# Kernel tuning notes

Hardware: AMD Instinct MI355X
Metric: run time of the kernel (lower is better)

## Reference

```python
import jax, jax.numpy as jnp
import numpy as np

NEG_INF = -9e15
NEG_SLOPE = 0.2

def setup_inputs() -> dict:
    key = jax.random.key(0)
    k1, k2, k3, k4 = jax.random.split(key, 4)
    N, d_in, d_out = 8192, 256, 256
    x = jax.random.normal(k1, (N, d_in), dtype=jnp.float32)
    adj = jax.random.randint(k2, (N, N), 0, 2).astype(jnp.float32)
    W = jax.random.normal(k3, (d_in, d_out), dtype=jnp.float32) * (1.0 / np.sqrt(d_in))
    a = jax.random.normal(k4, (2 * d_out,), dtype=jnp.float32) * (1.0 / np.sqrt(2 * d_out))
    return {"x": x, "adj": adj, "W": W, "a": a}

def reference(x, adj, W, a):
    d_out = W.shape[1]
    Wh = x @ W                                   # [N, d_out]
    # a([Wh_i || Wh_j]) decomposed: e_ij = <a_src, Wh_i> + <a_dst, Wh_j>
    e_src = Wh @ a[:d_out]                       # [N]
    e_dst = Wh @ a[d_out:]                       # [N]
    e = jax.nn.leaky_relu(e_src[:, None] + e_dst[None, :], NEG_SLOPE)  # [N, N]
    N = Wh.shape[0]
    mask = (adj > 0) | jnp.eye(N, dtype=bool)
    e = jnp.where(mask, e, NEG_INF)
    alpha = jax.nn.softmax(e, axis=1)            # [N, N]
    h = alpha @ Wh                               # [N, d_out]
    return h
```

## Files before the change

kernel.cpp:

```cpp
#include <hip/hip_runtime.h>
#include <stdint.h>

#define N 8192
#define D 256

typedef __attribute__((ext_vector_type(4))) float f32x4;
typedef __attribute__((ext_vector_type(8))) short bf16x8;

__device__ __forceinline__ unsigned short f2bf(float f) {
    unsigned u = __float_as_uint(f);
    u += 0x7fff + ((u >> 16) & 1);
    return (unsigned short)(u >> 16);
}
__device__ __forceinline__ float leaky(float x) {
    return fmaxf(x, 0.f) + 0.2f * fminf(x, 0.f);
}
__device__ __forceinline__ void sync_lds() {
    asm volatile("s_waitcnt lgkmcnt(0)\n\ts_barrier" ::: "memory");
}

#define K1_BM 16
__global__ __launch_bounds__(256) void k1_gemm(const float* __restrict__ x,
                                               const float* __restrict__ W,
                                               float* __restrict__ Wh,
                                               unsigned short* __restrict__ WhT) {
    __shared__ float xsT[32][20];
    const int t = threadIdx.x;
    const int r0 = blockIdx.x * K1_BM;
    float acc[K1_BM];
#pragma unroll
    for (int i = 0; i < K1_BM; ++i) acc[i] = 0.f;

    for (int k0 = 0; k0 < D; k0 += 32) {
        __syncthreads();
        if (t < 128) {
            int r = t >> 3, ks = (t & 7) * 4;
            float4 v = *(const float4*)(x + (size_t)(r0 + r) * D + k0 + ks);
            xsT[ks + 0][r] = v.x; xsT[ks + 1][r] = v.y;
            xsT[ks + 2][r] = v.z; xsT[ks + 3][r] = v.w;
        }
        __syncthreads();
#pragma unroll 8
        for (int kk = 0; kk < 32; ++kk) {
            float wv = W[(size_t)(k0 + kk) * D + t];
#pragma unroll
            for (int rc = 0; rc < K1_BM / 4; ++rc) {
                float4 xv = *(const float4*)&xsT[kk][rc * 4];
                acc[rc * 4 + 0] += xv.x * wv;
                acc[rc * 4 + 1] += xv.y * wv;
                acc[rc * 4 + 2] += xv.z * wv;
                acc[rc * 4 + 3] += xv.w * wv;
            }
        }
    }
#pragma unroll
    for (int r = 0; r < K1_BM; ++r) Wh[(size_t)(r0 + r) * D + t] = acc[r];
    unsigned short pk[K1_BM];
#pragma unroll
    for (int r = 0; r < K1_BM; ++r) pk[r] = f2bf(acc[r]);
    uint4* dst = (uint4*)(WhT + (size_t)t * N + r0);
    dst[0] = *(uint4*)&pk[0];
    dst[1] = *(uint4*)&pk[8];
}

__global__ __launch_bounds__(256) void k2_edot(const float* __restrict__ Wh,
                                               const float* __restrict__ a,
                                               float* __restrict__ e_src,
                                               float* __restrict__ e_dst) {
    const int wave = threadIdx.x >> 6, lane = threadIdx.x & 63;
    const int row = blockIdx.x * 4 + wave;
    float4 wv = *(const float4*)(Wh + (size_t)row * D + lane * 4);
    float4 as = *(const float4*)(a + lane * 4);
    float4 ad = *(const float4*)(a + D + lane * 4);
    float ps = wv.x * as.x + wv.y * as.y + wv.z * as.z + wv.w * as.w;
    float pd = wv.x * ad.x + wv.y * ad.y + wv.z * ad.z + wv.w * ad.w;
#pragma unroll
    for (int m = 1; m < 64; m <<= 1) {
        ps += __shfl_xor(ps, m);
        pd += __shfl_xor(pd, m);
    }
    if (lane == 0) { e_src[row] = ps; e_dst[row] = pd; }
}

__global__ __launch_bounds__(256) void k3_max(const float* __restrict__ e_dst,
                                              float* __restrict__ maxdst) {
    __shared__ float red[4];
    const int t = threadIdx.x;
    float m = -3.4e38f;
    for (int i = t; i < N; i += 256) m = fmaxf(m, e_dst[i]);
#pragma unroll
    for (int msk = 1; msk < 64; msk <<= 1) m = fmaxf(m, __shfl_xor(m, msk));
    if ((t & 63) == 0) red[t >> 6] = m;
    __syncthreads();
    if (t == 0) *maxdst = fmaxf(fmaxf(red[0], red[1]), fmaxf(red[2], red[3]));
}

#define BM 64
#define BK 64
#define RB (N / BM)
#define SPLITS 8
#define NITER ((N / SPLITS) / BK)
#define PSTRIDE 72
__global__ __launch_bounds__(512, 4) void k4_main(const float* __restrict__ adj,
                                                  const unsigned short* __restrict__ WhT,
                                                  const float* __restrict__ e_src,
                                                  const float* __restrict__ e_dst,
                                                  const float* __restrict__ maxdst,
                                                  float* __restrict__ O_part,
                                                  float* __restrict__ l_part) {
    __shared__ unsigned short p_lds[2][BM][PSTRIDE];

    const int t = threadIdx.x;
    const int rb = blockIdx.x & (RB - 1);
    const int s  = blockIdx.x >> 7;
    const int r0 = rb * BM;
    const int j0 = s * (N / SPLITS);

    const int pr = t >> 3;
    const int pc = (t & 7) * 8;
    const int gr = r0 + pr;

    const int w = t >> 6;
    const int lane = t & 63;
    const int quad = lane >> 4, lo = lane & 15;

    const float md = *maxdst;
    const float es = e_src[gr];
    const float m = leaky(es + md);

    f32x4 acc[4][2];
#pragma unroll
    for (int mt = 0; mt < 4; ++mt)
#pragma unroll
        for (int nt = 0; nt < 2; ++nt)
            acc[mt][nt] = (f32x4){0.f, 0.f, 0.f, 0.f};
    float lsum = 0.f;

    const float* adj_row = adj + (size_t)gr * N + j0 + pc;
    const float* ed_row  = e_dst + j0 + pc;
    const unsigned short* wt_base = WhT + (size_t)(w * 32 + lo) * N + j0 + quad * 8;

    float4 adjv0, adjv1, edv0, edv1;
    bf16x8 bfr[2][2];

    adjv0 = *(const float4*)(adj_row);
    adjv1 = *(const float4*)(adj_row + 4);
    edv0  = *(const float4*)(ed_row);
    edv1  = *(const float4*)(ed_row + 4);
#pragma unroll
    for (int ks2 = 0; ks2 < 2; ++ks2)
#pragma unroll
        for (int nt = 0; nt < 2; ++nt)
            bfr[ks2][nt] = *(const bf16x8*)(wt_base + (size_t)nt * (16 * N) + ks2 * 32);

    auto stage = [&](int its, int buf) {
        const int jb = j0 + its * BK + pc;
        float av[8] = {adjv0.x, adjv0.y, adjv0.z, adjv0.w,
                       adjv1.x, adjv1.y, adjv1.z, adjv1.w};
        float ev[8] = {edv0.x, edv0.y, edv0.z, edv0.w,
                       edv1.x, edv1.y, edv1.z, edv1.w};
        unsigned short pk[8];
#pragma unroll
        for (int jj = 0; jj < 8; ++jj) {
            float e = leaky(es + ev[jj]);
            bool keep = (av[jj] > 0.f) || (jb + jj == gr);
            float p = keep ? __expf(e - m) : 0.f;
            lsum += p;
            pk[jj] = f2bf(p);
        }
        *(uint4*)&p_lds[buf][pr][pc] = *(uint4*)pk;
    };

    stage(0, 0);
    adjv0 = *(const float4*)(adj_row + BK);
    adjv1 = *(const float4*)(adj_row + BK + 4);
    edv0  = *(const float4*)(ed_row + BK);
    edv1  = *(const float4*)(ed_row + BK + 4);
    sync_lds();

#pragma unroll 2
    for (int it = 0; it < NITER; ++it) {
        const int cb = it & 1, nb = cb ^ 1;

#pragma unroll
        for (int ks2 = 0; ks2 < 2; ++ks2) {
            bf16x8 afr[4];
#pragma unroll
            for (int mt = 0; mt < 4; ++mt)
                afr[mt] = *(const bf16x8*)&p_lds[cb][mt * 16 + lo][ks2 * 32 + quad * 8];
#pragma unroll
            for (int nt = 0; nt < 2; ++nt)
#pragma unroll
                for (int mt = 0; mt < 4; ++mt)
                    acc[mt][nt] = __builtin_amdgcn_mfma_f32_16x16x32_bf16(
                        afr[mt], bfr[ks2][nt], acc[mt][nt], 0, 0, 0);
        }

        {
            const int itn = (it + 1 < NITER) ? it + 1 : NITER - 1;
#pragma unroll
            for (int ks2 = 0; ks2 < 2; ++ks2)
#pragma unroll
                for (int nt = 0; nt < 2; ++nt)
                    bfr[ks2][nt] = *(const bf16x8*)(wt_base + (size_t)nt * (16 * N) +
                                                    itn * BK + ks2 * 32);
        }

        if (it + 1 < NITER) {
            stage(it + 1, nb);
            const int itn2 = (it + 2 < NITER) ? it + 2 : NITER - 1;
            adjv0 = *(const float4*)(adj_row + itn2 * BK);
            adjv1 = *(const float4*)(adj_row + itn2 * BK + 4);
            edv0  = *(const float4*)(ed_row + itn2 * BK);
            edv1  = *(const float4*)(ed_row + itn2 * BK + 4);
        }
        sync_lds();
    }

#pragma unroll
    for (int msk = 1; msk < 8; msk <<= 1) lsum += __shfl_xor(lsum, msk);
    if ((t & 7) == 0) l_part[(size_t)s * N + gr] = lsum;

#pragma unroll
    for (int mt = 0; mt < 4; ++mt) {
#pragma unroll
        for (int nt = 0; nt < 2; ++nt) {
            f32x4 v = acc[mt][nt];
            int col = w * 32 + nt * 16 + lo;
#pragma unroll
            for (int reg = 0; reg < 4; ++reg) {
                int row = mt * 16 + quad * 4 + reg;
                O_part[((size_t)s * N + r0 + row) * D + col] = v[reg];
            }
        }
    }
}

__global__ __launch_bounds__(256) void k5_reduce(const float* __restrict__ O_part,
                                                 const float* __restrict__ l_part,
                                                 float* __restrict__ out) {
    const int idx = blockIdx.x * 256 + threadIdx.x;
    const int r = idx >> 6;
    float lsum = 0.f;
#pragma unroll
    for (int s = 0; s < SPLITS; ++s) lsum += l_part[(size_t)s * N + r];
    f32x4 o = (f32x4){0.f, 0.f, 0.f, 0.f};
#pragma unroll
    for (int s = 0; s < SPLITS; ++s)
        o += *(const f32x4*)(O_part + (size_t)s * N * D + (size_t)idx * 4);
    const float inv = 1.f / lsum;
    *(f32x4*)(out + (size_t)idx * 4) = o * inv;
}

extern "C" void kernel_launch(void* const* d_in, const int* in_sizes, int n_in,
                              void* d_out, int out_size, void* d_ws, size_t ws_size,
                              hipStream_t stream) {
    const float* x   = (const float*)d_in[0];
    const float* adj = (const float*)d_in[1];
    const float* W   = (const float*)d_in[2];
    const float* a   = (const float*)d_in[3];
    float* out = (float*)d_out;

    char* ws = (char*)d_ws;
    float* Wh            = (float*)(ws);
    unsigned short* WhT  = (unsigned short*)(ws + 8388608);
    float* e_src         = (float*)(ws + 12582912);
    float* e_dst         = (float*)(ws + 12615680);
    float* maxdst        = (float*)(ws + 12648448);
    float* l_part        = (float*)(ws + 12648704);
    float* O_part        = (float*)(ws + 16777216);

    k1_gemm<<<N / K1_BM, 256, 0, stream>>>(x, W, Wh, WhT);
    k2_edot<<<N / 4, 256, 0, stream>>>(Wh, a, e_src, e_dst);
    k3_max<<<1, 256, 0, stream>>>(e_dst, maxdst);
    k4_main<<<RB * SPLITS, 512, 0, stream>>>(adj, WhT, e_src, e_dst, maxdst, O_part, l_part);
    k5_reduce<<<N * D / 4 / 256, 256, 0, stream>>>(O_part, l_part, out);
}
```

Baseline: 482.8 us.

## Precompress adjacency into a bitmask before the fused attention kernel

Adds a pre-pass kernel that reads the float adjacency matrix and packs it, with the self-loop diagonal folded in, into a 1-bit-per-entry mask. The main attention kernel then loads one mask byte per 8 columns instead of two float4 adjacency loads, and drops the per-element diagonal compare. The aim is to cut per-thread global load volume and register pressure in the main loop. The full adjacency matrix is still read once, now in a separate launch, and the mask is written and read back, so total memory traffic rises slightly.

```diff
diff --git a/kernel.cpp b/kernel.cpp
--- a/kernel.cpp
+++ b/kernel.cpp
@@ -17,6 +17,25 @@
 }
 __device__ __forceinline__ void sync_lds() {
     asm volatile("s_waitcnt lgkmcnt(0)\n\ts_barrier" ::: "memory");
+}
+
+__global__ __launch_bounds__(256) void k0_compress(const float* __restrict__ adj,
+                                                   unsigned int* __restrict__ mask) {
+    const int idx = blockIdx.x * 256 + threadIdx.x;
+    const int r = idx >> 8;
+    const int ww = idx & 255;
+    const float* src = adj + ((size_t)idx << 5);
+    unsigned int bits = 0;
+#pragma unroll
+    for (int j = 0; j < 8; ++j) {
+        float4 v = *(const float4*)(src + j * 4);
+        bits |= (v.x > 0.f ? 1u : 0u) << (j * 4 + 0);
+        bits |= (v.y > 0.f ? 1u : 0u) << (j * 4 + 1);
+        bits |= (v.z > 0.f ? 1u : 0u) << (j * 4 + 2);
+        bits |= (v.w > 0.f ? 1u : 0u) << (j * 4 + 3);
+    }
+    if ((r >> 5) == ww) bits |= 1u << (r & 31);
+    mask[idx] = bits;
 }
 
 #define K1_BM 16
@@ -101,7 +120,7 @@
 #define SPLITS 8
 #define NITER ((N / SPLITS) / BK)
 #define PSTRIDE 72
-__global__ __launch_bounds__(512, 4) void k4_main(const float* __restrict__ adj,
+__global__ __launch_bounds__(512, 4) void k4_main(const unsigned char* __restrict__ mask,
                                                   const unsigned short* __restrict__ WhT,
                                                   const float* __restrict__ e_src,
                                                   const float* __restrict__ e_dst,
@@ -117,7 +136,8 @@
     const int j0 = s * (N / SPLITS);
 
     const int pr = t >> 3;
-    const int pc = (t & 7) * 8;
+    const int pcw = t & 7;
+    const int pc = pcw * 8;
     const int gr = r0 + pr;
 
     const int w = t >> 6;
@@ -136,46 +156,41 @@
             acc[mt][nt] = (f32x4){0.f, 0.f, 0.f, 0.f};
     float lsum = 0.f;
 
-    const float* adj_row = adj + (size_t)gr * N + j0 + pc;
-    const float* ed_row  = e_dst + j0 + pc;
+    const unsigned char* mrow = mask + (size_t)gr * (N / 8) + (j0 >> 3) + pcw;
+    const float* ed_row = e_dst + j0 + pc;
     const unsigned short* wt_base = WhT + (size_t)(w * 32 + lo) * N + j0 + quad * 8;
 
-    float4 adjv0, adjv1, edv0, edv1;
+    unsigned int mb;
+    float4 edv0, edv1;
     bf16x8 bfr[2][2];
 
-    adjv0 = *(const float4*)(adj_row);
-    adjv1 = *(const float4*)(adj_row + 4);
-    edv0  = *(const float4*)(ed_row);
-    edv1  = *(const float4*)(ed_row + 4);
+    mb = mrow[0];
+    edv0 = *(const float4*)(ed_row);
+    edv1 = *(const float4*)(ed_row + 4);
 #pragma unroll
     for (int ks2 = 0; ks2 < 2; ++ks2)
 #pragma unroll
         for (int nt = 0; nt < 2; ++nt)
             bfr[ks2][nt] = *(const bf16x8*)(wt_base + (size_t)nt * (16 * N) + ks2 * 32);
 
-    auto stage = [&](int its, int buf) {
-        const int jb = j0 + its * BK + pc;
-        float av[8] = {adjv0.x, adjv0.y, adjv0.z, adjv0.w,
-                       adjv1.x, adjv1.y, adjv1.z, adjv1.w};
+    auto stage = [&](int buf) {
         float ev[8] = {edv0.x, edv0.y, edv0.z, edv0.w,
                        edv1.x, edv1.y, edv1.z, edv1.w};
         unsigned short pk[8];
 #pragma unroll
         for (int jj = 0; jj < 8; ++jj) {
             float e = leaky(es + ev[jj]);
-            bool keep = (av[jj] > 0.f) || (jb + jj == gr);
-            float p = keep ? __expf(e - m) : 0.f;
+            float p = ((mb >> jj) & 1u) ? __expf(e - m) : 0.f;
             lsum += p;
             pk[jj] = f2bf(p);
         }
         *(uint4*)&p_lds[buf][pr][pc] = *(uint4*)pk;
     };
 
-    stage(0, 0);
-    adjv0 = *(const float4*)(adj_row + BK);
-    adjv1 = *(const float4*)(adj_row + BK + 4);
-    edv0  = *(const float4*)(ed_row + BK);
-    edv1  = *(const float4*)(ed_row + BK + 4);
+    stage(0);
+    mb = mrow[8];
+    edv0 = *(const float4*)(ed_row + BK);
+    edv1 = *(const float4*)(ed_row + BK + 4);
     sync_lds();
 
 #pragma unroll 2
@@ -207,12 +222,11 @@
         }
 
         if (it + 1 < NITER) {
-            stage(it + 1, nb);
+            stage(nb);
             const int itn2 = (it + 2 < NITER) ? it + 2 : NITER - 1;
-            adjv0 = *(const float4*)(adj_row + itn2 * BK);
-            adjv1 = *(const float4*)(adj_row + itn2 * BK + 4);
-            edv0  = *(const float4*)(ed_row + itn2 * BK);
-            edv1  = *(const float4*)(ed_row + itn2 * BK + 4);
+            mb = mrow[itn2 * 8];
+            edv0 = *(const float4*)(ed_row + itn2 * BK);
+            edv1 = *(const float4*)(ed_row + itn2 * BK + 4);
         }
         sync_lds();
     }
@@ -268,11 +282,14 @@
     float* e_dst         = (float*)(ws + 12615680);
     float* maxdst        = (float*)(ws + 12648448);
     float* l_part        = (float*)(ws + 12648704);
-    float* O_part        = (float*)(ws + 16777216);
-
+    unsigned int* mask   = (unsigned int*)(ws + 13631488);
+    float* O_part        = (float*)(ws + 25165824);
+
+    k0_compress<<<N * N / 32 / 256, 256, 0, stream>>>(adj, mask);
     k1_gemm<<<N / K1_BM, 256, 0, stream>>>(x, W, Wh, WhT);
     k2_edot<<<N / 4, 256, 0, stream>>>(Wh, a, e_src, e_dst);
     k3_max<<<1, 256, 0, stream>>>(e_dst, maxdst);
-    k4_main<<<RB * SPLITS, 512, 0, stream>>>(adj, WhT, e_src, e_dst, maxdst, O_part, l_part);
+    k4_main<<<RB * SPLITS, 512, 0, stream>>>((const unsigned char*)mask, WhT, e_src, e_dst,
+                                             maxdst, O_part, l_part);
     k5_reduce<<<N * D / 4 / 256, 256, 0, stream>>>(O_part, l_part, out);
 }
```

Result: slower. 501.9 us (+3.9%).
